# Optimization experiments

Hardware: AMD Instinct MI355X
Metric: run time of the kernel (lower is better)

Reference implementation:

```python
import jax, jax.numpy as jnp
import numpy as np

B, N, F = 16, 1024, 256
HEADS, K, DOUT = 8, 512, 256
TAU = 1.0
EPS = 1e-08


def setup_inputs() -> dict:
    key = jax.random.key(0)
    k1, k2, k3, k4, k5, k6 = jax.random.split(key, 6)
    return {
        'Q': jax.random.normal(k1, (B, N, F), dtype=jnp.float32),
        'keys': jax.random.uniform(k2, (HEADS, K, F), dtype=jnp.float32),
        'conv_w': jax.random.normal(k3, (HEADS,), dtype=jnp.float32),
        'lin_w': jax.random.normal(k4, (DOUT, F), dtype=jnp.float32) * 0.05,
        'lin_b': jax.random.normal(k5, (DOUT,), dtype=jnp.float32) * 0.05,
        'mask': jax.random.randint(k6, (B, N), 0, 2, dtype=jnp.int32),
    }


def kl_reg(C):
    # C: (B, N, K)
    P = C ** 2
    cn = jnp.sum(C, axis=-2, keepdims=True) + EPS          # sum over N
    P = P / cn
    pn = jnp.sum(P, axis=-1, keepdims=True) + EPS          # sum over K
    P = P / pn
    kl = jnp.sum(P * (jnp.log(P + EPS) - jnp.log(C + EPS)))
    return 100.0 * kl


def memconv_fwd(Q, keys, conv_w, lin_w, lin_b, fmask):
    # pairwise L2 distance Q (B,N,F) vs keys (H,K,F) -> C (B,H,N,K)
    q2 = jnp.sum(Q * Q, axis=-1)                            # (B,N)
    k2 = jnp.sum(keys * keys, axis=-1)                      # (H,K)
    qk = jnp.einsum('bnf,hkf->bhnk', Q, keys)               # (B,H,N,K)
    d2 = q2[:, None, :, None] + k2[None, :, None, :] - 2.0 * qk
    C = jnp.sqrt(jnp.maximum(d2, 0.0))
    em = fmask[:, None, :, None]                            # (B,1,N,1) broadcast
    C = C * em
    # student-t kernel (gmn variant)
    C = (1.0 + C ** 2 / TAU) ** (-(0.5 * TAU + 0.5))
    C = C / jnp.sum(C, axis=-1, keepdims=True)
    C = C * em
    # conv1x1 over heads -> (B,N,K)
    C = jnp.einsum('bhnk,h->bnk', C, conv_w)
    C = jax.nn.softmax(C, axis=-1)
    C = C * fmask[:, :, None]
    kl = kl_reg(C)
    V = jnp.einsum('bnk,bnf->bkf', C, Q)                    # (B,K,F)
    out = jax.nn.leaky_relu(jnp.einsum('bkf,of->bko', V, lin_w) + lin_b, 0.01)
    return out, kl


def reference(Q, keys, conv_w, lin_w, lin_b, mask):
    fmask = mask.astype(Q.dtype)
    return memconv_fwd(Q, keys, conv_w, lin_w, lin_b, fmask)
```

## Files before the change

kernel.cpp:

```cpp
#include <hip/hip_runtime.h>
#include <math.h>

#define Bc 16
#define Nc 1024
#define Fc 256
#define Hc 8
#define Kc 512
#define DOUTc 256
#define EPSc 1e-8f

typedef short v8s __attribute__((ext_vector_type(8)));
typedef float v4f __attribute__((ext_vector_type(4)));

__device__ __forceinline__ float waveReduceSum(float v) {
    v += __shfl_xor(v, 32); v += __shfl_xor(v, 16); v += __shfl_xor(v, 8);
    v += __shfl_xor(v, 4);  v += __shfl_xor(v, 2);  v += __shfl_xor(v, 1);
    return v;
}

__device__ __forceinline__ unsigned short f2bf(float f) {
    unsigned int u = __float_as_uint(f);
    u = (u + 0x7fffu + ((u >> 16) & 1u)) >> 16;
    return (unsigned short)u;
}

__device__ __forceinline__ void lds_barrier() {
    __builtin_amdgcn_s_waitcnt(0xC07F);
    __builtin_amdgcn_s_barrier();
}

__global__ __launch_bounds__(256) void prep_all(
    const float* __restrict__ Q, const float* __restrict__ keys,
    const float* __restrict__ lin_w,
    float* __restrict__ k2g, unsigned short* __restrict__ Kp,
    unsigned short* __restrict__ Qbp, unsigned short* __restrict__ Wp,
    float* __restrict__ cn, float* __restrict__ klout) {
    __shared__ unsigned short T2[32][66];
    const int bx = blockIdx.x;
    const int tid = threadIdx.x;
    if (bx < 64) {
        int wv = tid >> 6, l = tid & 63;
#pragma unroll 4
        for (int rr = 0; rr < 16; rr++) {
            int row = bx * 64 + wv * 16 + rr;
            float4 v = *(const float4*)(keys + (size_t)row * Fc + l * 4);
            float s = v.x * v.x + v.y * v.y + v.z * v.z + v.w * v.w;
            s = waveReduceSum(s);
            if (l == 0) k2g[row] = s + 1.0f;
        }
    } else if (bx < 576) {
        int t = (bx - 64) * 256 + tid;
        int lane = t & 63, ci = t >> 6;
        int ct = ci & 7, ks = (ci >> 3) & 7, wv = (ci >> 6) & 3, h = ci >> 8;
        int qd = lane >> 4, li = lane & 15;
        int col = h * 512 + wv * 128 + ct * 16 + li;
        const float* src = keys + (size_t)col * Fc + ks * 32 + qd * 8;
        float4 a = *(const float4*)src;
        float4 b = *(const float4*)(src + 4);
        *(ushort4*)(Kp + (size_t)t * 8) = make_ushort4(f2bf(a.x), f2bf(a.y), f2bf(a.z), f2bf(a.w));
        *(ushort4*)(Kp + (size_t)t * 8 + 4) = make_ushort4(f2bf(b.x), f2bf(b.y), f2bf(b.z), f2bf(b.w));
    } else if (bx < 2624) {
        int i = bx - 576;
        int n0 = (i & 31) * 32, f0 = ((i >> 5) & 3) * 64, bb = i >> 7;
        {
            int n_l = tid >> 3, f_l = (tid & 7) * 8;
            const float* src = Q + ((size_t)(bb * Nc + n0 + n_l)) * Fc + f0 + f_l;
            float4 a = *(const float4*)src;
            float4 b = *(const float4*)(src + 4);
            T2[n_l][f_l + 0] = f2bf(a.x); T2[n_l][f_l + 1] = f2bf(a.y);
            T2[n_l][f_l + 2] = f2bf(a.z); T2[n_l][f_l + 3] = f2bf(a.w);
            T2[n_l][f_l + 4] = f2bf(b.x); T2[n_l][f_l + 5] = f2bf(b.y);
            T2[n_l][f_l + 6] = f2bf(b.z); T2[n_l][f_l + 7] = f2bf(b.w);
        }
        __syncthreads();
        int c = tid >> 6, L = tid & 63;
        int qd = L >> 4, li = L & 15;
        unsigned short o[8];
#pragma unroll
        for (int j = 0; j < 8; j++) o[j] = T2[qd * 8 + j][c * 16 + li];
        size_t idx = ((((size_t)bb * 16 + (f0 >> 4) + c) * 32 + (n0 >> 5)) * 64 + L) * 8;
        *(ushort4*)(Qbp + idx) = make_ushort4(o[0], o[1], o[2], o[3]);
        *(ushort4*)(Qbp + idx + 4) = make_ushort4(o[4], o[5], o[6], o[7]);
    } else if (bx < 2656) {
        int t = (bx - 2624) * 256 + tid;
        int lane = t & 63, ci = t >> 6;
        int ot = ci >> 3, fs = ci & 7;
        int qd = lane >> 4, li = lane & 15;
        const float* src = lin_w + (size_t)(ot * 16 + li) * Fc + fs * 32 + qd * 8;
        float4 a = *(const float4*)src;
        float4 b = *(const float4*)(src + 4);
        *(ushort4*)(Wp + (size_t)t * 8) = make_ushort4(f2bf(a.x), f2bf(a.y), f2bf(a.z), f2bf(a.w));
        *(ushort4*)(Wp + (size_t)t * 8 + 4) = make_ushort4(f2bf(b.x), f2bf(b.y), f2bf(b.z), f2bf(b.w));
    } else {
        int i = (bx - 2656) * 256 + tid;
        float4 z = make_float4(0.f, 0.f, 0.f, 0.f);
        float4* d = (float4*)(cn + (size_t)i * 16);
        d[0] = z; d[1] = z; d[2] = z; d[3] = z;
        if (bx == 2656 && tid == 0) *klout = 0.f;
    }
}

__global__ __launch_bounds__(256, 2) void cmfma_kernel(
    const float* __restrict__ Q, const unsigned short* __restrict__ Kp,
    const float* __restrict__ k2g, const float* __restrict__ conv_w,
    const int* __restrict__ mask, float* __restrict__ C,
    float* __restrict__ cn, unsigned short* __restrict__ Ctp) {
    __shared__ __align__(16) char uni[36864];
    __shared__ float q2h[4][16];
    __shared__ float msh[32];
    __shared__ float redb[Hc][4][32];
    __shared__ float mslot[4][32];
    __shared__ float eslot[4][32];
    float* k2s = (float*)uni;
    short* Ash = (short*)(uni + 16384);
    short (*Tb)[36] = (short (*)[36])uni;

    const int tid = threadIdx.x;
    const int wv = tid >> 6, L = tid & 63;
    const int qd = L >> 4, li = L & 15;
    const int gr0 = blockIdx.x * 32;
    const int b = gr0 >> 10;

    {
        int s_ = wv >> 1;
        int ksbase = (wv & 1) * 4;
        const float* qrow = Q + (size_t)(gr0 + s_ * 16 + li) * Fc + qd * 8;
        float q2part = 0.f;
#pragma unroll
        for (int j = 0; j < 4; j++) {
            int ks = ksbase + j;
            float4 a = *(const float4*)(qrow + ks * 32);
            float4 bq = *(const float4*)(qrow + ks * 32 + 4);
            v8s f;
            f[0] = (short)f2bf(a.x);  f[1] = (short)f2bf(a.y);
            f[2] = (short)f2bf(a.z);  f[3] = (short)f2bf(a.w);
            f[4] = (short)f2bf(bq.x); f[5] = (short)f2bf(bq.y);
            f[6] = (short)f2bf(bq.z); f[7] = (short)f2bf(bq.w);
            *(v8s*)&Ash[(((s_ * 8 + ks) * 64) + L) * 8] = f;
            q2part += a.x * a.x + a.y * a.y + a.z * a.z + a.w * a.w +
                      bq.x * bq.x + bq.y * bq.y + bq.z * bq.z + bq.w * bq.w;
        }
        q2part += __shfl_xor(q2part, 16);
        q2part += __shfl_xor(q2part, 32);
        if (qd == 0) q2h[wv][li] = q2part;
    }
    if (tid < 32) msh[tid] = (float)mask[gr0 + tid];
    for (int i = tid; i < Hc * Kc / 4; i += 256)
        *(float4*)&k2s[i * 4] = *(const float4*)(k2g + i * 4);

    v4f D[2][8], S[2][8];
#pragma unroll
    for (int s = 0; s < 2; s++)
#pragma unroll
        for (int ct = 0; ct < 8; ct++) {
            D[s][ct] = (v4f){0.f, 0.f, 0.f, 0.f};
            S[s][ct] = (v4f){0.f, 0.f, 0.f, 0.f};
        }

    const unsigned short* kwbase = Kp + (size_t)L * 8;
    v8s Bc0[8], Bn[8];
    {
        const unsigned short* p0 = kwbase + (size_t)(wv * 64) * 512;
#pragma unroll
        for (int ct = 0; ct < 8; ct++) Bc0[ct] = *(const v8s*)(p0 + ct * 512);
    }

    lds_barrier();

    float q2r[2][4], mrow[2][4];
#pragma unroll
    for (int s = 0; s < 2; s++)
#pragma unroll
        for (int r = 0; r < 4; r++) {
            q2r[s][r] = q2h[2 * s][qd * 4 + r] + q2h[2 * s + 1][qd * 4 + r];
            mrow[s][r] = msh[s * 16 + qd * 4 + r];
        }

#define LD_A(s, kk) (*(const v8s*)&Ash[(((s) * 8 + (kk)) * 64 + L) * 8])

    v8s Ac0 = LD_A(0, 0);
    v8s Ac1 = LD_A(1, 0);

#define KSTEP(kk, CUR, NXT)                                                        \
    do {                                                                           \
        int hn = h * 8 + (kk) + 1;                                                 \
        int hh = (hn >> 3) & 7, kn = hn & 7;                                       \
        const unsigned short* pb =                                                 \
            kwbase + (size_t)(((hh * 4 + wv) * 64 + kn * 8)) * 512;                \
        _Pragma("unroll") for (int ct = 0; ct < 8; ct++)                           \
            NXT[ct] = *(const v8s*)(pb + ct * 512);                                \
        v8s An0 = LD_A(0, ((kk) + 1) & 7);                                         \
        v8s An1 = LD_A(1, ((kk) + 1) & 7);                                         \
        __builtin_amdgcn_s_setprio(1);                                             \
        _Pragma("unroll") for (int ct = 0; ct < 8; ct++)                           \
            D[0][ct] = __builtin_amdgcn_mfma_f32_16x16x32_bf16(Ac0, CUR[ct],       \
                                                               D[0][ct], 0, 0, 0);\
        _Pragma("unroll") for (int ct = 0; ct < 8; ct++)                           \
            D[1][ct] = __builtin_amdgcn_mfma_f32_16x16x32_bf16(Ac1, CUR[ct],       \
                                                               D[1][ct], 0, 0, 0);\
        __builtin_amdgcn_s_setprio(0);                                             \
        Ac0 = An0; Ac1 = An1;                                                      \
    } while (0)

    for (int h = 0; h < Hc; ++h) {
        KSTEP(0, Bc0, Bn); KSTEP(1, Bn, Bc0);
        KSTEP(2, Bc0, Bn); KSTEP(3, Bn, Bc0);
        KSTEP(4, Bc0, Bn); KSTEP(5, Bn, Bc0);
        KSTEP(6, Bc0, Bn); KSTEP(7, Bn, Bc0);

        float rs[2][4] = {{0.f, 0.f, 0.f, 0.f}, {0.f, 0.f, 0.f, 0.f}};
#pragma unroll
        for (int ct = 0; ct < 8; ct++) {
            float k2v = k2s[h * Kc + wv * 128 + ct * 16 + li];
#pragma unroll
            for (int s = 0; s < 2; s++)
#pragma unroll
                for (int r = 0; r < 4; r++) {
                    float x = fmaf(-2.f, D[s][ct][r], q2r[s][r] + k2v);
                    float t = __builtin_amdgcn_rcpf(fmaxf(x, 1.0f));
                    D[s][ct][r] = t;
                    rs[s][r] += t;
                }
        }
#pragma unroll
        for (int s = 0; s < 2; s++)
#pragma unroll
            for (int r = 0; r < 4; r++) {
                rs[s][r] += __shfl_xor(rs[s][r], 1, 16);
                rs[s][r] += __shfl_xor(rs[s][r], 2, 16);
                rs[s][r] += __shfl_xor(rs[s][r], 4, 16);
                rs[s][r] += __shfl_xor(rs[s][r], 8, 16);
            }
        if (li == 0) {
#pragma unroll
            for (int s = 0; s < 2; s++)
#pragma unroll
                for (int r = 0; r < 4; r++) redb[h][wv][s * 16 + qd * 4 + r] = rs[s][r];
        }
        lds_barrier();
        float wh = conv_w[h];
        float sc[2][4];
#pragma unroll
        for (int s = 0; s < 2; s++)
#pragma unroll
            for (int r = 0; r < 4; r++) {
                int rw = s * 16 + qd * 4 + r;
                float tot = redb[h][0][rw] + redb[h][1][rw] + redb[h][2][rw] + redb[h][3][rw];
                sc[s][r] = wh * __builtin_amdgcn_rcpf(tot);
            }
#pragma unroll
        for (int s = 0; s < 2; s++)
#pragma unroll
            for (int ct = 0; ct < 8; ct++)
#pragma unroll
                for (int r = 0; r < 4; r++) {
                    S[s][ct][r] += sc[s][r] * D[s][ct][r];
                    D[s][ct][r] = 0.f;
                }
    }
#undef KSTEP
#undef LD_A

    float mx[2][4] = {{-1e30f, -1e30f, -1e30f, -1e30f}, {-1e30f, -1e30f, -1e30f, -1e30f}};
#pragma unroll
    for (int s = 0; s < 2; s++)
#pragma unroll
        for (int ct = 0; ct < 8; ct++)
#pragma unroll
            for (int r = 0; r < 4; r++) mx[s][r] = fmaxf(mx[s][r], S[s][ct][r]);
#pragma unroll
    for (int s = 0; s < 2; s++)
#pragma unroll
        for (int r = 0; r < 4; r++) {
            mx[s][r] = fmaxf(mx[s][r], __shfl_xor(mx[s][r], 1, 16));
            mx[s][r] = fmaxf(mx[s][r], __shfl_xor(mx[s][r], 2, 16));
            mx[s][r] = fmaxf(mx[s][r], __shfl_xor(mx[s][r], 4, 16));
            mx[s][r] = fmaxf(mx[s][r], __shfl_xor(mx[s][r], 8, 16));
        }
    if (li == 0) {
#pragma unroll
        for (int s = 0; s < 2; s++)
#pragma unroll
            for (int r = 0; r < 4; r++) mslot[wv][s * 16 + qd * 4 + r] = mx[s][r];
    }
    lds_barrier();
#pragma unroll
    for (int s = 0; s < 2; s++)
#pragma unroll
        for (int r = 0; r < 4; r++) {
            int rw = s * 16 + qd * 4 + r;
            mx[s][r] = fmaxf(fmaxf(mslot[0][rw], mslot[1][rw]),
                             fmaxf(mslot[2][rw], mslot[3][rw]));
        }
    float es[2][4] = {{0.f, 0.f, 0.f, 0.f}, {0.f, 0.f, 0.f, 0.f}};
#pragma unroll
    for (int s = 0; s < 2; s++)
#pragma unroll
        for (int ct = 0; ct < 8; ct++)
#pragma unroll
            for (int r = 0; r < 4; r++) {
                float e = __expf(S[s][ct][r] - mx[s][r]);
                S[s][ct][r] = e;
                es[s][r] += e;
            }
#pragma unroll
    for (int s = 0; s < 2; s++)
#pragma unroll
        for (int r = 0; r < 4; r++) {
            es[s][r] += __shfl_xor(es[s][r], 1, 16);
            es[s][r] += __shfl_xor(es[s][r], 2, 16);
            es[s][r] += __shfl_xor(es[s][r], 4, 16);
            es[s][r] += __shfl_xor(es[s][r], 8, 16);
        }
    if (li == 0) {
#pragma unroll
        for (int s = 0; s < 2; s++)
#pragma unroll
            for (int r = 0; r < 4; r++) eslot[wv][s * 16 + qd * 4 + r] = es[s][r];
    }
    lds_barrier();
    float inv[2][4];
#pragma unroll
    for (int s = 0; s < 2; s++)
#pragma unroll
        for (int r = 0; r < 4; r++) {
            int rw = s * 16 + qd * 4 + r;
            float tot = eslot[0][rw] + eslot[1][rw] + eslot[2][rw] + eslot[3][rw];
            inv[s][r] = mrow[s][r] / tot;
        }
#pragma unroll
    for (int ct = 0; ct < 8; ct++) {
        int k = wv * 128 + ct * 16 + li;
        float colsum = 0.f;
#pragma unroll
        for (int s = 0; s < 2; s++) {
            float cv[4];
#pragma unroll
            for (int r = 0; r < 4; r++) {
                cv[r] = S[s][ct][r] * inv[s][r];
                C[(size_t)(gr0 + s * 16 + qd * 4 + r) * Kc + k] = cv[r];
                colsum += cv[r];
            }
            short4 t4;
            t4.x = (short)f2bf(cv[0]); t4.y = (short)f2bf(cv[1]);
            t4.z = (short)f2bf(cv[2]); t4.w = (short)f2bf(cv[3]);
            *(short4*)&Tb[k][s * 16 + qd * 4] = t4;
        }
        colsum += __shfl_xor(colsum, 16);
        colsum += __shfl_xor(colsum, 32);
        if (qd == 0) atomicAdd(&cn[b * Kc + k], colsum);
    }
    lds_barrier();
    {
        const int ns0 = (gr0 & 1023) >> 5;
#pragma unroll
        for (int kk = 0; kk < 2; kk++) {
            int k = tid * 2 + kk;
            int kt = k >> 4, klo = k & 15;
            size_t cbase = (((size_t)b * 32 + kt) * 32 + ns0) * 512;
#pragma unroll
            for (int q2i = 0; q2i < 4; q2i++) {
                short4 lo = *(short4*)&Tb[k][q2i * 8];
                short4 hi = *(short4*)&Tb[k][q2i * 8 + 4];
                short4* d = (short4*)(Ctp + cbase + (size_t)(q2i * 16 + klo) * 8);
                d[0] = lo; d[1] = hi;
            }
        }
    }
}

__global__ __launch_bounds__(256) void klv_kernel(
    const unsigned short* __restrict__ Ctp, const unsigned short* __restrict__ Qbp,
    unsigned short* __restrict__ Vp, const float* __restrict__ C,
    const float* __restrict__ cn, float* __restrict__ klout) {
    __shared__ short Vt[64][76];
    __shared__ float red[4];
    int tid = threadIdx.x;
    int bx = blockIdx.x;
    if (bx < 512) {
        int w = tid >> 6, L = tid & 63;
        int qd = L >> 4, li = L & 15;
        int wr = w >> 1, wc = w & 1;
        int bb = bx >> 5;
        int rem = bx & 31;
        int ktb = rem >> 2, ftb = rem & 3;
        int KT0 = ktb * 4 + wr * 2;
        int FT0 = ftb * 4 + wc * 2;
        const unsigned short* pa0 = Ctp + (((size_t)bb * 32 + KT0) * 32) * 512 + L * 8;
        const unsigned short* pa1 = pa0 + (size_t)32 * 512;
        const unsigned short* pb0 = Qbp + (((size_t)bb * 16 + FT0) * 32) * 512 + L * 8;
        const unsigned short* pb1 = pb0 + (size_t)32 * 512;
        v4f acc[2][2];
#pragma unroll
        for (int a = 0; a < 2; a++)
#pragma unroll
            for (int c = 0; c < 2; c++) acc[a][c] = (v4f){0.f, 0.f, 0.f, 0.f};

        v8s Ae0 = *(const v8s*)pa0, Ae1 = *(const v8s*)pa1;
        v8s Be0 = *(const v8s*)pb0, Be1 = *(const v8s*)pb1;
        v8s Ao0 = *(const v8s*)(pa0 + 512), Ao1 = *(const v8s*)(pa1 + 512);
        v8s Bo0 = *(const v8s*)(pb0 + 512), Bo1 = *(const v8s*)(pb1 + 512);
        for (int ns = 0; ns < 32; ns += 2) {
            int n2 = (ns + 2) & 31;
            int n3 = (ns + 3) & 31;
            acc[0][0] = __builtin_amdgcn_mfma_f32_16x16x32_bf16(Ae0, Be0, acc[0][0], 0, 0, 0);
            acc[0][1] = __builtin_amdgcn_mfma_f32_16x16x32_bf16(Ae0, Be1, acc[0][1], 0, 0, 0);
            acc[1][0] = __builtin_amdgcn_mfma_f32_16x16x32_bf16(Ae1, Be0, acc[1][0], 0, 0, 0);
            acc[1][1] = __builtin_amdgcn_mfma_f32_16x16x32_bf16(Ae1, Be1, acc[1][1], 0, 0, 0);
            Ae0 = *(const v8s*)(pa0 + n2 * 512); Ae1 = *(const v8s*)(pa1 + n2 * 512);
            Be0 = *(const v8s*)(pb0 + n2 * 512); Be1 = *(const v8s*)(pb1 + n2 * 512);
            acc[0][0] = __builtin_amdgcn_mfma_f32_16x16x32_bf16(Ao0, Bo0, acc[0][0], 0, 0, 0);
            acc[0][1] = __builtin_amdgcn_mfma_f32_16x16x32_bf16(Ao0, Bo1, acc[0][1], 0, 0, 0);
            acc[1][0] = __builtin_amdgcn_mfma_f32_16x16x32_bf16(Ao1, Bo0, acc[1][0], 0, 0, 0);
            acc[1][1] = __builtin_amdgcn_mfma_f32_16x16x32_bf16(Ao1, Bo1, acc[1][1], 0, 0, 0);
            Ao0 = *(const v8s*)(pa0 + n3 * 512); Ao1 = *(const v8s*)(pa1 + n3 * 512);
            Bo0 = *(const v8s*)(pb0 + n3 * 512); Bo1 = *(const v8s*)(pb1 + n3 * 512);
        }
#pragma unroll
        for (int a = 0; a < 2; a++)
#pragma unroll
            for (int c = 0; c < 2; c++)
#pragma unroll
                for (int r = 0; r < 4; r++)
                    Vt[(wr * 2 + a) * 16 + qd * 4 + r][(wc * 2 + c) * 16 + li] =
                        (short)f2bf(acc[a][c][r]);
        __syncthreads();
        {
            int ci = tid >> 5, s5 = tid & 31;
            int mtl = ci >> 1, fsl = ci & 1;
            size_t mt_g = (size_t)bb * 32 + ktb * 4 + mtl;
            size_t fs_g = (size_t)ftb * 2 + fsl;
#pragma unroll
            for (int half = 0; half < 2; half++) {
                int L2 = s5 + half * 32;
                int qd2 = L2 >> 4, li2 = L2 & 15;
                short4 x0 = *(short4*)&Vt[mtl * 16 + li2][fsl * 32 + qd2 * 8];
                short4 x1 = *(short4*)&Vt[mtl * 16 + li2][fsl * 32 + qd2 * 8 + 4];
                short4* d = (short4*)(Vp + ((mt_g * 8 + fs_g) * 64 + L2) * 8);
                d[0] = x0; d[1] = x1;
            }
        }
    } else {
        int bk = bx - 512;
        int w = tid >> 6, l = tid & 63;
        int b0 = (bk * 16) >> 10;
        const float* np = cn + b0 * Kc + l * 8;
        v4f n0 = *(const v4f*)np;
        v4f n1 = *(const v4f*)(np + 4);
        float rn[8];
#pragma unroll
        for (int j = 0; j < 4; j++) {
            rn[j] = __builtin_amdgcn_rcpf(n0[j] + EPSc);
            rn[4 + j] = __builtin_amdgcn_rcpf(n1[j] + EPSc);
        }
        float kacc = 0.f;
#pragma unroll
        for (int rr = 0; rr < 4; rr++) {
            int row = bk * 16 + w * 4 + rr;
            const float* cp = C + (size_t)row * Kc + l * 8;
            v4f c0 = *(const v4f*)cp;
            v4f c1 = *(const v4f*)(cp + 4);
            float cc[8] = {c0[0], c0[1], c0[2], c0[3], c1[0], c1[1], c1[2], c1[3]};
            float p[8];
#pragma unroll
            for (int j = 0; j < 8; j++) p[j] = cc[j] * cc[j] * rn[j];
            float s = p[0] + p[1] + p[2] + p[3] + p[4] + p[5] + p[6] + p[7];
            float pn = waveReduceSum(s) + EPSc;
            float rpn = __builtin_amdgcn_rcpf(pn);
#pragma unroll
            for (int j = 0; j < 8; j++) {
                float P = p[j] * rpn;
                kacc += P * __logf((P + EPSc) * __builtin_amdgcn_rcpf(cc[j] + EPSc));
            }
        }
        kacc = waveReduceSum(kacc);
        if (l == 0) red[w] = kacc;
        __syncthreads();
        if (tid == 0)
            atomicAdd(klout, 100.f * (red[0] + red[1] + red[2] + red[3]));
    }
}

__global__ __launch_bounds__(256) void ofma_kernel(
    const unsigned short* __restrict__ Vp, const unsigned short* __restrict__ Wp,
    const float* __restrict__ bias, float* __restrict__ out) {
    int tid = threadIdx.x;
    int w = tid >> 6, L = tid & 63;
    int qd = L >> 4, li = L & 15;
    int wr = w >> 1, wc = w & 1;
    int MT0 = blockIdx.x * 4 + wr * 2;
    int OT0 = blockIdx.y * 4 + wc * 2;
    const unsigned short* pa0 = Vp + ((size_t)MT0 * 8) * 512 + L * 8;
    const unsigned short* pa1 = pa0 + (size_t)8 * 512;
    const unsigned short* pb0 = Wp + ((size_t)OT0 * 8) * 512 + L * 8;
    const unsigned short* pb1 = pb0 + (size_t)8 * 512;
    v4f acc[2][2];
#pragma unroll
    for (int a = 0; a < 2; a++)
#pragma unroll
        for (int c = 0; c < 2; c++) acc[a][c] = (v4f){0.f, 0.f, 0.f, 0.f};
    v8s Ae0 = *(const v8s*)pa0, Ae1 = *(const v8s*)pa1;
    v8s Be0 = *(const v8s*)pb0, Be1 = *(const v8s*)pb1;
    v8s Ao0 = *(const v8s*)(pa0 + 512), Ao1 = *(const v8s*)(pa1 + 512);
    v8s Bo0 = *(const v8s*)(pb0 + 512), Bo1 = *(const v8s*)(pb1 + 512);
#pragma unroll
    for (int fs = 0; fs < 8; fs += 2) {
        int n2 = (fs + 2) & 7;
        int n3 = (fs + 3) & 7;
        acc[0][0] = __builtin_amdgcn_mfma_f32_16x16x32_bf16(Ae0, Be0, acc[0][0], 0, 0, 0);
        acc[0][1] = __builtin_amdgcn_mfma_f32_16x16x32_bf16(Ae0, Be1, acc[0][1], 0, 0, 0);
        acc[1][0] = __builtin_amdgcn_mfma_f32_16x16x32_bf16(Ae1, Be0, acc[1][0], 0, 0, 0);
        acc[1][1] = __builtin_amdgcn_mfma_f32_16x16x32_bf16(Ae1, Be1, acc[1][1], 0, 0, 0);
        Ae0 = *(const v8s*)(pa0 + n2 * 512); Ae1 = *(const v8s*)(pa1 + n2 * 512);
        Be0 = *(const v8s*)(pb0 + n2 * 512); Be1 = *(const v8s*)(pb1 + n2 * 512);
        acc[0][0] = __builtin_amdgcn_mfma_f32_16x16x32_bf16(Ao0, Bo0, acc[0][0], 0, 0, 0);
        acc[0][1] = __builtin_amdgcn_mfma_f32_16x16x32_bf16(Ao0, Bo1, acc[0][1], 0, 0, 0);
        acc[1][0] = __builtin_amdgcn_mfma_f32_16x16x32_bf16(Ao1, Bo0, acc[1][0], 0, 0, 0);
        acc[1][1] = __builtin_amdgcn_mfma_f32_16x16x32_bf16(Ao1, Bo1, acc[1][1], 0, 0, 0);
        Ao0 = *(const v8s*)(pa0 + n3 * 512); Ao1 = *(const v8s*)(pa1 + n3 * 512);
        Bo0 = *(const v8s*)(pb0 + n3 * 512); Bo1 = *(const v8s*)(pb1 + n3 * 512);
    }
#pragma unroll
    for (int c = 0; c < 2; c++) {
        float bv = bias[(OT0 + c) * 16 + li];
#pragma unroll
        for (int a = 0; a < 2; a++)
#pragma unroll
            for (int r = 0; r < 4; r++) {
                int m = (MT0 + a) * 16 + qd * 4 + r;
                int o = (OT0 + c) * 16 + li;
                float x = acc[a][c][r] + bv;
                out[(size_t)m * DOUTc + o] = x > 0.f ? x : 0.01f * x;
            }
    }
}

extern "C" void kernel_launch(void* const* d_in, const int* in_sizes, int n_in,
                              void* d_out, int out_size, void* d_ws, size_t ws_size,
                              hipStream_t stream) {
    const float* Q = (const float*)d_in[0];
    const float* keys = (const float*)d_in[1];
    const float* conv_w = (const float*)d_in[2];
    const float* lin_w = (const float*)d_in[3];
    const float* lin_b = (const float*)d_in[4];
    const int* mask = (const int*)d_in[5];

    float* out = (float*)d_out;
    float* kl = out + (size_t)Bc * Kc * DOUTc;

    float* ws = (float*)d_ws;
    float* C = ws;
    float* k2 = C + (size_t)Bc * Nc * Kc;
    float* cn = k2 + (size_t)Hc * Kc;
    unsigned short* Kp = (unsigned short*)(cn + (size_t)Bc * Kc);
    unsigned short* Ctp = Kp + (size_t)Hc * Kc * Fc;
    unsigned short* Qbp = Ctp + (size_t)Bc * Nc * Kc;
    unsigned short* Vp = Qbp + (size_t)Bc * Nc * Fc;
    unsigned short* Wp = Vp + (size_t)Bc * Kc * Fc;

    prep_all<<<2658, 256, 0, stream>>>(Q, keys, lin_w, k2, Kp, Qbp, Wp, cn, kl);
    cmfma_kernel<<<Bc * Nc / 32, 256, 0, stream>>>(Q, Kp, k2, conv_w, mask, C, cn, Ctp);
    klv_kernel<<<1536, 256, 0, stream>>>(Ctp, Qbp, Vp, C, cn, kl);
    ofma_kernel<<<dim3(Bc * Kc / 64, DOUTc / 64), 256, 0, stream>>>(Vp, Wp, lin_b, out);
}
```

Measured before the change: 172.2 us.

## Retile distance MFMA kernel to 64 rows with 8 waves per block

The C-computation kernel now processes 64 query rows per block with 512 threads. Each wave computes a 4x4 tile of 16x16 MFMA outputs instead of 2x8, so each key fragment is reused across more rows. The kernel adds a deeper register pipeline for key fragments, reads k2 from global memory instead of LDS, and emits the transposed bf16 C in two passes. This is meant to cut key-fragment traffic per row and raise MFMA density. In exchange, wider cross-wave reductions, more barriers and higher register pressure could hurt occupancy.

```diff
diff --git a/kernel.cpp b/kernel.cpp
--- a/kernel.cpp
+++ b/kernel.cpp
@@ -100,25 +100,24 @@
     }
 }
 
-__global__ __launch_bounds__(256, 2) void cmfma_kernel(
+__global__ __launch_bounds__(512, 2) void cmfma_kernel(
     const float* __restrict__ Q, const unsigned short* __restrict__ Kp,
     const float* __restrict__ k2g, const float* __restrict__ conv_w,
     const int* __restrict__ mask, float* __restrict__ C,
     float* __restrict__ cn, unsigned short* __restrict__ Ctp) {
     __shared__ __align__(16) char uni[36864];
-    __shared__ float q2h[4][16];
-    __shared__ float msh[32];
-    __shared__ float redb[Hc][4][32];
-    __shared__ float mslot[4][32];
-    __shared__ float eslot[4][32];
-    float* k2s = (float*)uni;
-    short* Ash = (short*)(uni + 16384);
+    __shared__ float q2h[8][16];
+    __shared__ float msh[64];
+    __shared__ float redb[Hc][8][64];
+    __shared__ float mslot[8][64];
+    __shared__ float eslot[8][64];
+    short* Ash = (short*)uni;
     short (*Tb)[36] = (short (*)[36])uni;
 
     const int tid = threadIdx.x;
     const int wv = tid >> 6, L = tid & 63;
     const int qd = L >> 4, li = L & 15;
-    const int gr0 = blockIdx.x * 32;
+    const int gr0 = blockIdx.x * 64;
     const int b = gr0 >> 10;
 
     {
@@ -144,86 +143,90 @@
         q2part += __shfl_xor(q2part, 32);
         if (qd == 0) q2h[wv][li] = q2part;
     }
-    if (tid < 32) msh[tid] = (float)mask[gr0 + tid];
-    for (int i = tid; i < Hc * Kc / 4; i += 256)
-        *(float4*)&k2s[i * 4] = *(const float4*)(k2g + i * 4);
-
-    v4f D[2][8], S[2][8];
-#pragma unroll
-    for (int s = 0; s < 2; s++)
-#pragma unroll
-        for (int ct = 0; ct < 8; ct++) {
+    if (tid < 64) msh[tid] = (float)mask[gr0 + tid];
+
+    v4f D[4][4], S[4][4];
+#pragma unroll
+    for (int s = 0; s < 4; s++)
+#pragma unroll
+        for (int ct = 0; ct < 4; ct++) {
             D[s][ct] = (v4f){0.f, 0.f, 0.f, 0.f};
             S[s][ct] = (v4f){0.f, 0.f, 0.f, 0.f};
         }
 
     const unsigned short* kwbase = Kp + (size_t)L * 8;
-    v8s Bc0[8], Bn[8];
-    {
-        const unsigned short* p0 = kwbase + (size_t)(wv * 64) * 512;
-#pragma unroll
-        for (int ct = 0; ct < 8; ct++) Bc0[ct] = *(const v8s*)(p0 + ct * 512);
-    }
-
+    v8s Bb[4][4];
+
+#define BLOAD(slot, hn)                                                            \
+    do {                                                                           \
+        const unsigned short* pb =                                                 \
+            kwbase + (size_t)((((hn) >> 3) & 7) * 256 + (wv >> 1) * 64 +           \
+                              ((hn) & 7) * 8 + (wv & 1) * 4) * 512;                \
+        Bb[slot][0] = *(const v8s*)(pb);                                           \
+        Bb[slot][1] = *(const v8s*)(pb + 512);                                     \
+        Bb[slot][2] = *(const v8s*)(pb + 1024);                                    \
+        Bb[slot][3] = *(const v8s*)(pb + 1536);                                    \
+    } while (0)
+
+#define LDA(dst, kk2)                                                              \
+    do {                                                                           \
+        _Pragma("unroll") for (int s = 0; s < 4; s++)                              \
+            dst[s] = *(const v8s*)&Ash[((s * 8 + (kk2)) * 64 + L) * 8];            \
+    } while (0)
+
+    BLOAD(0, 0);
+    BLOAD(1, 1);
     lds_barrier();
-
-    float q2r[2][4], mrow[2][4];
-#pragma unroll
-    for (int s = 0; s < 2; s++)
-#pragma unroll
-        for (int r = 0; r < 4; r++) {
-            q2r[s][r] = q2h[2 * s][qd * 4 + r] + q2h[2 * s + 1][qd * 4 + r];
-            mrow[s][r] = msh[s * 16 + qd * 4 + r];
-        }
-
-#define LD_A(s, kk) (*(const v8s*)&Ash[(((s) * 8 + (kk)) * 64 + L) * 8])
-
-    v8s Ac0 = LD_A(0, 0);
-    v8s Ac1 = LD_A(1, 0);
-
-#define KSTEP(kk, CUR, NXT)                                                        \
+    v8s Aa[4], Ab[4];
+    LDA(Aa, 0);
+
+#define KSTEP(kk, ACUR, ANXT)                                                      \
     do {                                                                           \
-        int hn = h * 8 + (kk) + 1;                                                 \
-        int hh = (hn >> 3) & 7, kn = hn & 7;                                       \
-        const unsigned short* pb =                                                 \
-            kwbase + (size_t)(((hh * 4 + wv) * 64 + kn * 8)) * 512;                \
-        _Pragma("unroll") for (int ct = 0; ct < 8; ct++)                           \
-            NXT[ct] = *(const v8s*)(pb + ct * 512);                                \
-        v8s An0 = LD_A(0, ((kk) + 1) & 7);                                         \
-        v8s An1 = LD_A(1, ((kk) + 1) & 7);                                         \
+        BLOAD((kk + 2) & 3, h * 8 + kk + 2);                                       \
+        LDA(ANXT, ((kk) + 1) & 7);                                                 \
         __builtin_amdgcn_s_setprio(1);                                             \
-        _Pragma("unroll") for (int ct = 0; ct < 8; ct++)                           \
-            D[0][ct] = __builtin_amdgcn_mfma_f32_16x16x32_bf16(Ac0, CUR[ct],       \
-                                                               D[0][ct], 0, 0, 0);\
-        _Pragma("unroll") for (int ct = 0; ct < 8; ct++)                           \
-            D[1][ct] = __builtin_amdgcn_mfma_f32_16x16x32_bf16(Ac1, CUR[ct],       \
-                                                               D[1][ct], 0, 0, 0);\
+        _Pragma("unroll") for (int s = 0; s < 4; s++)                              \
+            _Pragma("unroll") for (int ct = 0; ct < 4; ct++)                       \
+                D[s][ct] = __builtin_amdgcn_mfma_f32_16x16x32_bf16(                \
+                    ACUR[s], Bb[(kk) & 3][ct], D[s][ct], 0, 0, 0);                 \
         __builtin_amdgcn_s_setprio(0);                                             \
-        Ac0 = An0; Ac1 = An1;                                                      \
+        ;                                                                          \
     } while (0)
 
     for (int h = 0; h < Hc; ++h) {
-        KSTEP(0, Bc0, Bn); KSTEP(1, Bn, Bc0);
-        KSTEP(2, Bc0, Bn); KSTEP(3, Bn, Bc0);
-        KSTEP(4, Bc0, Bn); KSTEP(5, Bn, Bc0);
-        KSTEP(6, Bc0, Bn); KSTEP(7, Bn, Bc0);
-
-        float rs[2][4] = {{0.f, 0.f, 0.f, 0.f}, {0.f, 0.f, 0.f, 0.f}};
-#pragma unroll
-        for (int ct = 0; ct < 8; ct++) {
-            float k2v = k2s[h * Kc + wv * 128 + ct * 16 + li];
-#pragma unroll
-            for (int s = 0; s < 2; s++)
+        KSTEP(0, Aa, Ab);
+        float k2r[4];
+#pragma unroll
+        for (int ct = 0; ct < 4; ct++)
+            k2r[ct] = k2g[h * Kc + wv * 64 + ct * 16 + li];
+        KSTEP(1, Ab, Aa); KSTEP(2, Aa, Ab); KSTEP(3, Ab, Aa);
+        KSTEP(4, Aa, Ab); KSTEP(5, Ab, Aa); KSTEP(6, Aa, Ab); KSTEP(7, Ab, Aa);
+
+        float rs[4][4];
+        v4f q2v[4];
+#pragma unroll
+        for (int s = 0; s < 4; s++) {
+            q2v[s] = *(const v4f*)&q2h[2 * s][qd * 4];
+            v4f t2 = *(const v4f*)&q2h[2 * s + 1][qd * 4];
+            q2v[s] += t2;
+#pragma unroll
+            for (int r = 0; r < 4; r++) rs[s][r] = 0.f;
+        }
+#pragma unroll
+        for (int ct = 0; ct < 4; ct++) {
+            float k2v = k2r[ct];
+#pragma unroll
+            for (int s = 0; s < 4; s++)
 #pragma unroll
                 for (int r = 0; r < 4; r++) {
-                    float x = fmaf(-2.f, D[s][ct][r], q2r[s][r] + k2v);
+                    float x = fmaf(-2.f, D[s][ct][r], q2v[s][r] + k2v);
                     float t = __builtin_amdgcn_rcpf(fmaxf(x, 1.0f));
                     D[s][ct][r] = t;
                     rs[s][r] += t;
                 }
         }
 #pragma unroll
-        for (int s = 0; s < 2; s++)
+        for (int s = 0; s < 4; s++)
 #pragma unroll
             for (int r = 0; r < 4; r++) {
                 rs[s][r] += __shfl_xor(rs[s][r], 1, 16);
@@ -233,139 +236,144 @@
             }
         if (li == 0) {
 #pragma unroll
-            for (int s = 0; s < 2; s++)
-#pragma unroll
-                for (int r = 0; r < 4; r++) redb[h][wv][s * 16 + qd * 4 + r] = rs[s][r];
+            for (int s = 0; s < 4; s++)
+#pragma unroll
+                for (int r = 0; r < 4; r++)
+                    redb[h][wv][s * 16 + qd * 4 + r] = rs[s][r];
         }
         lds_barrier();
         float wh = conv_w[h];
-        float sc[2][4];
-#pragma unroll
-        for (int s = 0; s < 2; s++)
+#pragma unroll
+        for (int s = 0; s < 4; s++) {
+            v4f tot = *(const v4f*)&redb[h][0][s * 16 + qd * 4];
+#pragma unroll
+            for (int w = 1; w < 8; w++) tot += *(const v4f*)&redb[h][w][s * 16 + qd * 4];
 #pragma unroll
             for (int r = 0; r < 4; r++) {
-                int rw = s * 16 + qd * 4 + r;
-                float tot = redb[h][0][rw] + redb[h][1][rw] + redb[h][2][rw] + redb[h][3][rw];
-                sc[s][r] = wh * __builtin_amdgcn_rcpf(tot);
-            }
-#pragma unroll
-        for (int s = 0; s < 2; s++)
-#pragma unroll
-            for (int ct = 0; ct < 8; ct++)
-#pragma unroll
-                for (int r = 0; r < 4; r++) {
-                    S[s][ct][r] += sc[s][r] * D[s][ct][r];
+                float sc = wh * __builtin_amdgcn_rcpf(tot[r]);
+#pragma unroll
+                for (int ct = 0; ct < 4; ct++) {
+                    S[s][ct][r] += sc * D[s][ct][r];
                     D[s][ct][r] = 0.f;
                 }
+            }
+        }
     }
 #undef KSTEP
-#undef LD_A
-
-    float mx[2][4] = {{-1e30f, -1e30f, -1e30f, -1e30f}, {-1e30f, -1e30f, -1e30f, -1e30f}};
-#pragma unroll
-    for (int s = 0; s < 2; s++)
-#pragma unroll
-        for (int ct = 0; ct < 8; ct++)
-#pragma unroll
-            for (int r = 0; r < 4; r++) mx[s][r] = fmaxf(mx[s][r], S[s][ct][r]);
-#pragma unroll
-    for (int s = 0; s < 2; s++)
+#undef LDA
+#undef BLOAD
+
+    float mx[4][4];
+#pragma unroll
+    for (int s = 0; s < 4; s++)
 #pragma unroll
         for (int r = 0; r < 4; r++) {
-            mx[s][r] = fmaxf(mx[s][r], __shfl_xor(mx[s][r], 1, 16));
-            mx[s][r] = fmaxf(mx[s][r], __shfl_xor(mx[s][r], 2, 16));
-            mx[s][r] = fmaxf(mx[s][r], __shfl_xor(mx[s][r], 4, 16));
-            mx[s][r] = fmaxf(mx[s][r], __shfl_xor(mx[s][r], 8, 16));
+            float m = S[s][0][r];
+            m = fmaxf(m, S[s][1][r]); m = fmaxf(m, S[s][2][r]); m = fmaxf(m, S[s][3][r]);
+            m = fmaxf(m, __shfl_xor(m, 1, 16));
+            m = fmaxf(m, __shfl_xor(m, 2, 16));
+            m = fmaxf(m, __shfl_xor(m, 4, 16));
+            m = fmaxf(m, __shfl_xor(m, 8, 16));
+            mx[s][r] = m;
         }
     if (li == 0) {
 #pragma unroll
-        for (int s = 0; s < 2; s++)
+        for (int s = 0; s < 4; s++)
 #pragma unroll
             for (int r = 0; r < 4; r++) mslot[wv][s * 16 + qd * 4 + r] = mx[s][r];
     }
     lds_barrier();
 #pragma unroll
-    for (int s = 0; s < 2; s++)
+    for (int s = 0; s < 4; s++) {
+        v4f m = *(const v4f*)&mslot[0][s * 16 + qd * 4];
+#pragma unroll
+        for (int w = 1; w < 8; w++) {
+            v4f t = *(const v4f*)&mslot[w][s * 16 + qd * 4];
+#pragma unroll
+            for (int r = 0; r < 4; r++) m[r] = fmaxf(m[r], t[r]);
+        }
+#pragma unroll
+        for (int r = 0; r < 4; r++) mx[s][r] = m[r];
+    }
+    float es[4][4];
+#pragma unroll
+    for (int s = 0; s < 4; s++)
 #pragma unroll
         for (int r = 0; r < 4; r++) {
-            int rw = s * 16 + qd * 4 + r;
-            mx[s][r] = fmaxf(fmaxf(mslot[0][rw], mslot[1][rw]),
-                             fmaxf(mslot[2][rw], mslot[3][rw]));
-        }
-    float es[2][4] = {{0.f, 0.f, 0.f, 0.f}, {0.f, 0.f, 0.f, 0.f}};
-#pragma unroll
-    for (int s = 0; s < 2; s++)
-#pragma unroll
-        for (int ct = 0; ct < 8; ct++)
-#pragma unroll
-            for (int r = 0; r < 4; r++) {
-                float e = __expf(S[s][ct][r] - mx[s][r]);
-                S[s][ct][r] = e;
-                es[s][r] += e;
-            }
-#pragma unroll
-    for (int s = 0; s < 2; s++)
-#pragma unroll
-        for (int r = 0; r < 4; r++) {
-            es[s][r] += __shfl_xor(es[s][r], 1, 16);
-            es[s][r] += __shfl_xor(es[s][r], 2, 16);
-            es[s][r] += __shfl_xor(es[s][r], 4, 16);
-            es[s][r] += __shfl_xor(es[s][r], 8, 16);
+            float e0 = __expf(S[s][0][r] - mx[s][r]);
+            float e1 = __expf(S[s][1][r] - mx[s][r]);
+            float e2 = __expf(S[s][2][r] - mx[s][r]);
+            float e3 = __expf(S[s][3][r] - mx[s][r]);
+            S[s][0][r] = e0; S[s][1][r] = e1; S[s][2][r] = e2; S[s][3][r] = e3;
+            float e = e0 + e1 + e2 + e3;
+            e += __shfl_xor(e, 1, 16);
+            e += __shfl_xor(e, 2, 16);
+            e += __shfl_xor(e, 4, 16);
+            e += __shfl_xor(e, 8, 16);
+            es[s][r] = e;
         }
     if (li == 0) {
 #pragma unroll
-        for (int s = 0; s < 2; s++)
+        for (int s = 0; s < 4; s++)
 #pragma unroll
             for (int r = 0; r < 4; r++) eslot[wv][s * 16 + qd * 4 + r] = es[s][r];
     }
     lds_barrier();
-    float inv[2][4];
-#pragma unroll
-    for (int s = 0; s < 2; s++)
-#pragma unroll
-        for (int r = 0; r < 4; r++) {
-            int rw = s * 16 + qd * 4 + r;
-            float tot = eslot[0][rw] + eslot[1][rw] + eslot[2][rw] + eslot[3][rw];
-            inv[s][r] = mrow[s][r] / tot;
-        }
-#pragma unroll
-    for (int ct = 0; ct < 8; ct++) {
-        int k = wv * 128 + ct * 16 + li;
-        float colsum = 0.f;
-#pragma unroll
-        for (int s = 0; s < 2; s++) {
-            float cv[4];
-#pragma unroll
-            for (int r = 0; r < 4; r++) {
-                cv[r] = S[s][ct][r] * inv[s][r];
-                C[(size_t)(gr0 + s * 16 + qd * 4 + r) * Kc + k] = cv[r];
-                colsum += cv[r];
-            }
-            short4 t4;
-            t4.x = (short)f2bf(cv[0]); t4.y = (short)f2bf(cv[1]);
-            t4.z = (short)f2bf(cv[2]); t4.w = (short)f2bf(cv[3]);
-            *(short4*)&Tb[k][s * 16 + qd * 4] = t4;
-        }
-        colsum += __shfl_xor(colsum, 16);
-        colsum += __shfl_xor(colsum, 32);
-        if (qd == 0) atomicAdd(&cn[b * Kc + k], colsum);
-    }
-    lds_barrier();
-    {
-        const int ns0 = (gr0 & 1023) >> 5;
-#pragma unroll
-        for (int kk = 0; kk < 2; kk++) {
-            int k = tid * 2 + kk;
-            int kt = k >> 4, klo = k & 15;
-            size_t cbase = (((size_t)b * 32 + kt) * 32 + ns0) * 512;
+    float inv[4][4];
+#pragma unroll
+    for (int s = 0; s < 4; s++) {
+        v4f tot = *(const v4f*)&eslot[0][s * 16 + qd * 4];
+#pragma unroll
+        for (int w = 1; w < 8; w++) tot += *(const v4f*)&eslot[w][s * 16 + qd * 4];
+        v4f mr = *(const v4f*)&msh[s * 16 + qd * 4];
+#pragma unroll
+        for (int r = 0; r < 4; r++) inv[s][r] = mr[r] / tot[r];
+    }
+
+    const int ns0 = (gr0 & 1023) >> 5;
+    float colsum[4] = {0.f, 0.f, 0.f, 0.f};
+#pragma unroll
+    for (int p = 0; p < 2; p++) {
+        if (p == 1) lds_barrier();
+#pragma unroll
+        for (int ct = 0; ct < 4; ct++) {
+            int k = wv * 64 + ct * 16 + li;
+#pragma unroll
+            for (int s2 = 0; s2 < 2; s2++) {
+                int s = p * 2 + s2;
+                float cv[4];
+#pragma unroll
+                for (int r = 0; r < 4; r++) {
+                    cv[r] = S[s][ct][r] * inv[s][r];
+                    C[(size_t)(gr0 + s * 16 + qd * 4 + r) * Kc + k] = cv[r];
+                    colsum[ct] += cv[r];
+                }
+                short4 t4;
+                t4.x = (short)f2bf(cv[0]); t4.y = (short)f2bf(cv[1]);
+                t4.z = (short)f2bf(cv[2]); t4.w = (short)f2bf(cv[3]);
+                *(short4*)&Tb[k][s2 * 16 + qd * 4] = t4;
+            }
+        }
+        lds_barrier();
+        {
+            int kt = tid >> 4, klo = tid & 15;
+            size_t cbase = (((size_t)b * 32 + kt) * 32 + ns0 + p) * 512;
 #pragma unroll
             for (int q2i = 0; q2i < 4; q2i++) {
-                short4 lo = *(short4*)&Tb[k][q2i * 8];
-                short4 hi = *(short4*)&Tb[k][q2i * 8 + 4];
+                short4 lo = *(short4*)&Tb[tid][q2i * 8];
+                short4 hi = *(short4*)&Tb[tid][q2i * 8 + 4];
                 short4* d = (short4*)(Ctp + cbase + (size_t)(q2i * 16 + klo) * 8);
                 d[0] = lo; d[1] = hi;
             }
         }
+    }
+#pragma unroll
+    for (int ct = 0; ct < 4; ct++) {
+        int k = wv * 64 + ct * 16 + li;
+        float cs = colsum[ct];
+        cs += __shfl_xor(cs, 16);
+        cs += __shfl_xor(cs, 32);
+        if (qd == 0) atomicAdd(&cn[b * Kc + k], cs);
     }
 }
 
@@ -559,7 +567,7 @@
     unsigned short* Wp = Vp + (size_t)Bc * Kc * Fc;
 
     prep_all<<<2658, 256, 0, stream>>>(Q, keys, lin_w, k2, Kp, Qbp, Wp, cn, kl);
-    cmfma_kernel<<<Bc * Nc / 32, 256, 0, stream>>>(Q, Kp, k2, conv_w, mask, C, cn, Ctp);
+    cmfma_kernel<<<Bc * Nc / 64, 512, 0, stream>>>(Q, Kp, k2, conv_w, mask, C, cn, Ctp);
     klv_kernel<<<1536, 256, 0, stream>>>(Ctp, Qbp, Vp, C, cn, kl);
     ofma_kernel<<<dim3(Bc * Kc / 64, DOUTc / 64), 256, 0, stream>>>(Vp, Wp, lin_b, out);
 }
```

Measured after the change: 175.6 us. No clear change (+1.9%).
